# Performance work log

Measured on AMD Instinct MI355X. Metric: run time of the kernel, lower is better.

## Reference

```python
import jax, jax.numpy as jnp
import numpy as np

H = 32       # num query heads
KVH = 8      # num kv heads
HD = 64      # head_dim
ROPE_BASE = 10000.0


def _rope_cos_sin(seq_len, dtype):
    # inv_freq over half the head dim, emb = cat(freqs, freqs)
    inv_freq = 1.0 / (ROPE_BASE ** (jnp.arange(0, HD, 2, dtype=jnp.float32) / HD))
    t = jnp.arange(seq_len, dtype=jnp.float32)
    freqs = t[:, None] * inv_freq[None, :]          # (S, HD/2)
    emb = jnp.concatenate([freqs, freqs], axis=-1)  # (S, HD)
    return jnp.cos(emb).astype(dtype), jnp.sin(emb).astype(dtype)


def _rotate(x):
    x1, x2 = x[..., : HD // 2], x[..., HD // 2 :]
    return jnp.concatenate([-x2, x1], axis=-1)


def setup_inputs() -> dict:
    key = jax.random.key(0)
    ks = jax.random.split(key, 9)
    B, T, D = 2, 2048, 2048
    kv_dim = KVH * HD
    s = 0.02
    return {
        "x": jax.random.normal(ks[0], (B, T, D), jnp.float32),
        "Wq": jax.random.normal(ks[1], (D, D), jnp.float32) * s,
        "bq": jax.random.normal(ks[2], (D,), jnp.float32) * s,
        "Wk": jax.random.normal(ks[3], (kv_dim, D), jnp.float32) * s,
        "bk": jax.random.normal(ks[4], (kv_dim,), jnp.float32) * s,
        "Wv": jax.random.normal(ks[5], (kv_dim, D), jnp.float32) * s,
        "bv": jax.random.normal(ks[6], (kv_dim,), jnp.float32) * s,
        "Wo": jax.random.normal(ks[7], (D, D), jnp.float32) * s,
        "bo": jax.random.normal(ks[8], (D,), jnp.float32) * s,
    }


def reference(x, Wq, bq, Wk, bk, Wv, bv, Wo, bo):
    B, T, D = x.shape
    S = T  # self-attention, no KV cache (offset = 0)

    # QKV projections
    q = (x @ Wq.T + bq).reshape(B, T, H, HD)
    k = (x @ Wk.T + bk).reshape(B, S, KVH, HD)
    v = (x @ Wv.T + bv).reshape(B, S, KVH, HD)

    # RoPE (rotary dim == head_dim, offset 0)
    cos, sin = _rope_cos_sin(S, q.dtype)
    cos = cos[None, :, None, :]  # (1, S, 1, HD)
    sin = sin[None, :, None, :]
    q = q * cos + _rotate(q) * sin
    k = k * cos + _rotate(k) * sin

    # GQA: repeat kv heads (repeat_interleave along head dim)
    r = H // KVH
    k = jnp.repeat(k, r, axis=2)  # (B, S, H, HD)
    v = jnp.repeat(v, r, axis=2)

    # causal scaled dot-product attention
    scale = 1.0 / np.sqrt(HD)
    scores = jnp.einsum("bthd,bshd->bhts", q, k) * scale  # (B, H, T, S)
    causal = jnp.tril(jnp.ones((T, S), dtype=bool))
    scores = jnp.where(causal[None, None], scores, jnp.finfo(scores.dtype).min)
    probs = jax.nn.softmax(scores.astype(jnp.float32), axis=-1).astype(q.dtype)
    attn = jnp.einsum("bhts,bshd->bthd", probs, v)  # (B, T, H, HD)

    out = attn.reshape(B, T, H * HD) @ Wo.T + bo
    return out
```

## Files before the change

### kernel.cpp

```cpp
#include <hip/hip_runtime.h>
#include <hip/hip_bf16.h>
#include <cstdint>

#define B_ 2
#define T_ 2048
#define D_ 2048
#define H_ 32
#define KVH_ 8
#define HD_ 64
#define NQKV_ 3072
#define M_ 4096

typedef __attribute__((ext_vector_type(8))) __bf16 bf16x8;
typedef __attribute__((ext_vector_type(4))) float f32x4;
typedef __attribute__((ext_vector_type(4))) uint32_t u32x4;

__device__ __forceinline__ uint16_t f2bf(float f) {
  uint32_t u = __builtin_bit_cast(uint32_t, f);
  return (uint16_t)((u + 0x7FFFu + ((u >> 16) & 1u)) >> 16);
}

__device__ __forceinline__ uint32_t cvt_pk(float lo, float hi) {
  uint32_t r;
  asm("v_cvt_pk_bf16_f32 %0, %1, %2" : "=v"(r) : "v"(lo), "v"(hi));
  return r;
}

__device__ __forceinline__ void gload_lds16(const void* g, void* l) {
  __builtin_amdgcn_global_load_lds(
      (const __attribute__((address_space(1))) void*)(uintptr_t)g,
      (__attribute__((address_space(3))) void*)(uintptr_t)l, 16, 0, 0);
}

__global__ void cvt_bf16_k(const float* __restrict__ in, uint16_t* __restrict__ out, int n) {
  int i = (blockIdx.x * 256 + threadIdx.x) * 8;
  if (i >= n) return;
  float4 a = *reinterpret_cast<const float4*>(in + i);
  float4 b = *reinterpret_cast<const float4*>(in + i + 4);
  uint4 v;
  v.x = (uint32_t)f2bf(a.x) | ((uint32_t)f2bf(a.y) << 16);
  v.y = (uint32_t)f2bf(a.z) | ((uint32_t)f2bf(a.w) << 16);
  v.z = (uint32_t)f2bf(b.x) | ((uint32_t)f2bf(b.y) << 16);
  v.w = (uint32_t)f2bf(b.z) | ((uint32_t)f2bf(b.w) << 16);
  *reinterpret_cast<uint4*>(out + i) = v;
}

__global__ void concat_bias_k(const float* __restrict__ bq, const float* __restrict__ bk,
                              const float* __restrict__ bv, float* __restrict__ out) {
  int i = blockIdx.x * 256 + threadIdx.x;
  if (i >= NQKV_) return;
  out[i] = (i < D_) ? bq[i] : (i < D_ + 512) ? bk[i - D_] : bv[i - D_ - 512];
}

__global__ void rope_tab_k(float* __restrict__ cosT, float* __restrict__ sinT) {
  int i = blockIdx.x * 256 + threadIdx.x;
  int d = i & 31;
  int t = i >> 5;
  float inv = expf(-(float)d * (1.0f / 32.0f) * logf(10000.0f));
  float f = (float)t * inv;
  cosT[i] = cosf(f);
  sinT[i] = sinf(f);
}

#define BM 128
#define BN 128
#define BK 64
__global__ __launch_bounds__(256, 3)
void gemm_bf16(const uint16_t* __restrict__ A, const uint16_t* __restrict__ Bw,
               const float* __restrict__ bias, float* __restrict__ C,
               int M, int N, int K) {
  __shared__ __align__(16) uint16_t As[BM * BK];
  __shared__ __align__(16) uint16_t Bs[BN * BK];
  const int tid = threadIdx.x;
  const int lane = tid & 63;
  const int w = tid >> 6;
  const int wm = w >> 1, wn = w & 1;
  const int l16 = lane & 15, lq = lane >> 4;

  int lin = blockIdx.y * gridDim.x + blockIdx.x;
  int qn = (gridDim.x * gridDim.y) >> 3;
  int swz = (lin & 7) * qn + (lin >> 3);
  const int m0 = (swz / gridDim.x) * BM, n0 = (swz % gridDim.x) * BN;

  f32x4 acc[4][4] = {};

  for (int k0 = 0; k0 < K; k0 += BK) {
#pragma unroll
    for (int r = 0; r < 4; ++r) {
      int idx = r * 256 + tid;
      int row = idx >> 3;
      int c8 = (idx & 7) ^ (row & 7);
      gload_lds16(A + (size_t)(m0 + row) * K + k0 + c8 * 8, &As[idx * 8]);
    }
#pragma unroll
    for (int r = 0; r < 4; ++r) {
      int idx = r * 256 + tid;
      int row = idx >> 3;
      int c8 = (idx & 7) ^ (row & 7);
      gload_lds16(Bw + (size_t)(n0 + row) * K + k0 + c8 * 8, &Bs[idx * 8]);
    }
    __syncthreads();
#pragma unroll
    for (int ks = 0; ks < 2; ++ks) {
      bf16x8 av[4], bv[4];
      int k8 = ks * 4 + lq;
#pragma unroll
      for (int mi = 0; mi < 4; ++mi) {
        int row = wm * 64 + mi * 16 + l16;
        av[mi] = *reinterpret_cast<const bf16x8*>(&As[row * BK + ((k8 ^ (row & 7)) * 8)]);
      }
#pragma unroll
      for (int ni = 0; ni < 4; ++ni) {
        int row = wn * 64 + ni * 16 + l16;
        bv[ni] = *reinterpret_cast<const bf16x8*>(&Bs[row * BK + ((k8 ^ (row & 7)) * 8)]);
      }
#pragma unroll
      for (int mi = 0; mi < 4; ++mi)
#pragma unroll
        for (int ni = 0; ni < 4; ++ni)
          acc[mi][ni] = __builtin_amdgcn_mfma_f32_16x16x32_bf16(av[mi], bv[ni], acc[mi][ni], 0, 0, 0);
    }
    __syncthreads();
  }

#pragma unroll
  for (int mi = 0; mi < 4; ++mi) {
    int r0 = m0 + wm * 64 + mi * 16 + lq * 4;
#pragma unroll
    for (int ni = 0; ni < 4; ++ni) {
      int c = n0 + wn * 64 + ni * 16 + l16;
      float bb = bias[c];
#pragma unroll
      for (int rr = 0; rr < 4; ++rr)
        C[(size_t)(r0 + rr) * N + c] = acc[mi][ni][rr] + bb;
    }
  }
}

__global__ void rope_qk_k(const float* __restrict__ QKV, const float* __restrict__ cosT,
                          const float* __restrict__ sinT, uint16_t* __restrict__ qb,
                          uint16_t* __restrict__ kb) {
  int tid = blockIdx.x * 256 + threadIdx.x;
  int d = tid & 31;
  int t = (tid >> 5) & (T_ - 1);
  int rest = tid >> 16;
  int hh = rest % 40;
  int b = rest / 40;
  const float PREQ = 0.125f * 1.44269504f;
  float c = cosT[t * 32 + d];
  float s = sinT[t * 32 + d];
  size_t rowoff = (size_t)(b * T_ + t) * NQKV_;
  const int lq = d >> 3, e = d & 7;
  const int l16 = t & 15;
  const int lofs = (lq * 16 + l16) * 8 + e;
  if (hh < H_) {
    const float* q = QKV + rowoff + hh * 64;
    float x1 = q[d], x2 = q[d + 32];
    int tile = t >> 5, mf = (t >> 4) & 1;
    size_t base = ((size_t)(b * H_ + hh) * 64 + tile) * 2048;
    qb[base + (0 * 2 + mf) * 512 + lofs] = f2bf((x1 * c - x2 * s) * PREQ);
    qb[base + (1 * 2 + mf) * 512 + lofs] = f2bf((x2 * c + x1 * s) * PREQ);
  } else {
    int kh = hh - H_;
    const float* kp = QKV + rowoff + D_ + kh * 64;
    float x1 = kp[d], x2 = kp[d + 32];
    int it = t >> 6, nf = (t >> 4) & 3;
    size_t base = (size_t)(b * KVH_ + kh) * (T_ * HD_) + (size_t)it * 4096;
    kb[base + (0 * 8 + nf) * 512 + lofs] = f2bf(x1 * c - x2 * s);
    kb[base + (4 + nf) * 512 + lofs] = f2bf(x2 * c + x1 * s);
  }
}

__global__ void cvt_v_k(const float* __restrict__ QKV, uint16_t* __restrict__ vt) {
  int tid = blockIdx.x * 256 + threadIdx.x;
  int t8 = tid & 255;
  int rest = tid >> 8;
  int b = rest >> 9;
  int col = 2560 + (rest & 511);
  int d = rest & 63;
  int kvh = (rest >> 6) & 7;
  uint16_t tmp[8];
#pragma unroll
  for (int i = 0; i < 8; ++i)
    tmp[i] = f2bf(QKV[(size_t)(b * T_ + t8 * 8 + i) * NQKV_ + col]);
  uint4 v;
  v.x = (uint32_t)tmp[0] | ((uint32_t)tmp[1] << 16);
  v.y = (uint32_t)tmp[2] | ((uint32_t)tmp[3] << 16);
  v.z = (uint32_t)tmp[4] | ((uint32_t)tmp[5] << 16);
  v.w = (uint32_t)tmp[6] | ((uint32_t)tmp[7] << 16);
  int it = t8 >> 3, k2 = (t8 >> 2) & 1, lq = t8 & 3;
  int dn = d >> 4, l16 = d & 15;
  size_t base = (size_t)(b * KVH_ + kvh) * (T_ * HD_);
  *reinterpret_cast<uint4*>(vt + base + ((size_t)(it * 2 + k2) * 4 + dn) * 512 +
                            (lq * 16 + l16) * 8) = v;
}

__global__ __launch_bounds__(256, 2)
void flash_attn_k(const uint16_t* __restrict__ qb, const uint16_t* __restrict__ kb,
                  const uint16_t* __restrict__ vt, uint16_t* __restrict__ ob) {
  __shared__ __align__(16) uint16_t P_lds[4][32 * 72];
  const int lane = threadIdx.x & 63;
  const int w = threadIdx.x >> 6;
  const int l16 = lane & 15, lq = lane >> 4;
  const int bh = (blockIdx.x & 15) * 4 + w;
  const int rank = blockIdx.x >> 4;
  const int pair = rank & 31;
  const int tile = (rank & 32) ? (63 - pair) : pair;
  const int b = bh >> 5, h = bh & 31;
  const int kvh = h >> 2;
  uint16_t* P = P_lds[w];

  const uint16_t* Qp = qb + ((size_t)(b * H_ + h) * 64 + tile) * 2048;
  const uint16_t* Kp = kb + (size_t)(b * KVH_ + kvh) * (T_ * HD_);
  const uint16_t* Vp = vt + (size_t)(b * KVH_ + kvh) * (T_ * HD_);
  const int lofs = lane * 8;

  const int q0 = tile * 32;
  u32x4 ones_u = {0x3F803F80u, 0x3F803F80u, 0x3F803F80u, 0x3F803F80u};
  bf16x8 ones = __builtin_bit_cast(bf16x8, ones_u);

  bf16x8 aq[2][2];
#pragma unroll
  for (int mf = 0; mf < 2; ++mf)
#pragma unroll
    for (int ks = 0; ks < 2; ++ks)
      aq[mf][ks] = *reinterpret_cast<const bf16x8*>(Qp + (ks * 2 + mf) * 512 + lofs);

  f32x4 acc[2][4] = {};
  f32x4 acc_l[2] = {};

  const int nt = (tile >> 1) + 1;

  bf16x8 kA[2][4], kB[2][4];
#pragma unroll
  for (int ks = 0; ks < 2; ++ks)
#pragma unroll
    for (int nf = 0; nf < 4; ++nf)
      kA[ks][nf] = *reinterpret_cast<const bf16x8*>(Kp + (ks * 4 + nf) * 512 + lofs);

#define FLASH_STEP(KCUR, KNXT, IT)                                                     \
  do {                                                                                 \
    const int kv0 = (IT) * 64;                                                         \
    f32x4 sacc[4][2] = {};                                                             \
    _Pragma("unroll")                                                                  \
    for (int ks = 0; ks < 2; ++ks)                                                     \
      _Pragma("unroll")                                                                \
      for (int nf = 0; nf < 4; ++nf)                                                   \
        _Pragma("unroll")                                                              \
        for (int mf = 0; mf < 2; ++mf)                                                 \
          sacc[nf][mf] = __builtin_amdgcn_mfma_f32_16x16x32_bf16(                      \
              KCUR[ks][nf], aq[mf][ks], sacc[nf][mf], 0, 0, 0);                        \
    const int itn = ((IT) + 1 < nt) ? (IT) + 1 : (IT);                                 \
    _Pragma("unroll")                                                                  \
    for (int ks = 0; ks < 2; ++ks)                                                     \
      _Pragma("unroll")                                                                \
      for (int nf = 0; nf < 4; ++nf)                                                   \
        KNXT[ks][nf] = *reinterpret_cast<const bf16x8*>(                               \
            Kp + ((size_t)(itn * 2 + ks) * 4 + nf) * 512 + lofs);                      \
    bf16x8 vv[2][4];                                                                   \
    _Pragma("unroll")                                                                  \
    for (int k2 = 0; k2 < 2; ++k2)                                                     \
      _Pragma("unroll")                                                                \
      for (int dn = 0; dn < 4; ++dn)                                                   \
        vv[k2][dn] = *reinterpret_cast<const bf16x8*>(                                 \
            Vp + ((size_t)((IT) * 2 + k2) * 4 + dn) * 512 + lofs);                     \
    if ((IT) == nt - 1) {                                                              \
      _Pragma("unroll")                                                                \
      for (int mf = 0; mf < 2; ++mf) {                                                 \
        int qg = q0 + mf * 16 + l16;                                                   \
        _Pragma("unroll")                                                              \
        for (int nf = 0; nf < 4; ++nf)                                                 \
          _Pragma("unroll")                                                            \
          for (int r = 0; r < 4; ++r)                                                  \
            if (kv0 + nf * 16 + lq * 4 + r > qg) sacc[nf][mf][r] = -1e30f;             \
      }                                                                                \
    }                                                                                  \
    _Pragma("unroll")                                                                  \
    for (int mf = 0; mf < 2; ++mf) {                                                   \
      uint16_t* rowp = P + (mf * 16 + l16) * 72;                                       \
      _Pragma("unroll")                                                                \
      for (int nf = 0; nf < 4; ++nf) {                                                 \
        float p0 = __builtin_amdgcn_exp2f(sacc[nf][mf][0]);                            \
        float p1 = __builtin_amdgcn_exp2f(sacc[nf][mf][1]);                            \
        float p2 = __builtin_amdgcn_exp2f(sacc[nf][mf][2]);                            \
        float p3 = __builtin_amdgcn_exp2f(sacc[nf][mf][3]);                            \
        uint2 pk;                                                                      \
        pk.x = cvt_pk(p0, p1);                                                         \
        pk.y = cvt_pk(p2, p3);                                                         \
        *reinterpret_cast<uint2*>(rowp + nf * 16 + lq * 4) = pk;                       \
      }                                                                                \
    }                                                                                  \
    bf16x8 pa[2][2];                                                                   \
    _Pragma("unroll")                                                                  \
    for (int mf = 0; mf < 2; ++mf)                                                     \
      _Pragma("unroll")                                                                \
      for (int k2 = 0; k2 < 2; ++k2)                                                   \
        pa[mf][k2] = *reinterpret_cast<const bf16x8*>(                                 \
            P + (mf * 16 + l16) * 72 + k2 * 32 + lq * 8);                              \
    _Pragma("unroll")                                                                  \
    for (int k2 = 0; k2 < 2; ++k2)                                                     \
      _Pragma("unroll")                                                                \
      for (int mf = 0; mf < 2; ++mf) {                                                 \
        acc_l[mf] = __builtin_amdgcn_mfma_f32_16x16x32_bf16(ones, pa[mf][k2],          \
                                                            acc_l[mf], 0, 0, 0);      \
        _Pragma("unroll")                                                              \
        for (int dn = 0; dn < 4; ++dn)                                                 \
          acc[mf][dn] = __builtin_amdgcn_mfma_f32_16x16x32_bf16(                       \
              vv[k2][dn], pa[mf][k2], acc[mf][dn], 0, 0, 0);                           \
      }                                                                                \
  } while (0)

  {
    int it = 0;
    for (;;) {
      FLASH_STEP(kA, kB, it);
      ++it;
      if (it == nt) break;
      FLASH_STEP(kB, kA, it);
      ++it;
      if (it == nt) break;
    }
  }
#undef FLASH_STEP

#pragma unroll
  for (int mf = 0; mf < 2; ++mf) {
    float inv = 1.0f / acc_l[mf][0];
    uint16_t* rowp = P + (mf * 16 + l16) * 72;
#pragma unroll
    for (int dn = 0; dn < 4; ++dn) {
      uint2 pk;
      pk.x = cvt_pk(acc[mf][dn][0] * inv, acc[mf][dn][1] * inv);
      pk.y = cvt_pk(acc[mf][dn][2] * inv, acc[mf][dn][3] * inv);
      *reinterpret_cast<uint2*>(rowp + dn * 16 + lq * 4) = pk;
    }
  }
  {
    int orow = lane >> 1, ohalf = (lane & 1) * 32;
    uint16_t* op = ob + (size_t)(b * T_ + q0 + orow) * D_ + h * HD_ + ohalf;
    const uint16_t* lp = P + orow * 72 + ohalf;
#pragma unroll
    for (int j = 0; j < 4; ++j)
      *reinterpret_cast<uint4*>(op + j * 8) = *reinterpret_cast<const uint4*>(lp + j * 8);
  }
}

extern "C" void kernel_launch(void* const* d_in, const int* in_sizes, int n_in,
                              void* d_out, int out_size, void* d_ws, size_t ws_size,
                              hipStream_t stream) {
  const float* x  = (const float*)d_in[0];
  const float* Wq = (const float*)d_in[1];
  const float* bq = (const float*)d_in[2];
  const float* Wk = (const float*)d_in[3];
  const float* bk = (const float*)d_in[4];
  const float* Wv = (const float*)d_in[5];
  const float* bv = (const float*)d_in[6];
  const float* Wo = (const float*)d_in[7];
  const float* bo = (const float*)d_in[8];
  float* out = (float*)d_out;

  char* ws = (char*)d_ws;
  size_t off = 0;
  auto alloc = [&](size_t bytes) {
    void* p = ws + off;
    off += (bytes + 255) & ~(size_t)255;
    return p;
  };
  uint16_t* xb    = (uint16_t*)alloc((size_t)M_ * D_ * 2);
  uint16_t* wqkv  = (uint16_t*)alloc((size_t)NQKV_ * D_ * 2);
  uint16_t* wo_b  = (uint16_t*)alloc((size_t)D_ * D_ * 2);
  float*    bqkv  = (float*)alloc(NQKV_ * 4);
  float*    cosT  = (float*)alloc(T_ * 32 * 4);
  float*    sinT  = (float*)alloc(T_ * 32 * 4);
  uint16_t* q_bf  = (uint16_t*)alloc((size_t)B_ * H_ * T_ * HD_ * 2);
  uint16_t* k_bf  = (uint16_t*)alloc((size_t)B_ * KVH_ * T_ * HD_ * 2);
  uint16_t* vt_bf = (uint16_t*)alloc((size_t)B_ * KVH_ * T_ * HD_ * 2);
  float*    qkvf  = (float*)alloc((size_t)M_ * NQKV_ * 4);
  uint16_t* attn_bf = (uint16_t*)qkvf;

  cvt_bf16_k<<<4096, 256, 0, stream>>>(x, xb, M_ * D_);
  cvt_bf16_k<<<2048, 256, 0, stream>>>(Wq, wqkv, D_ * D_);
  cvt_bf16_k<<<512, 256, 0, stream>>>(Wk, wqkv + (size_t)D_ * D_, 512 * D_);
  cvt_bf16_k<<<512, 256, 0, stream>>>(Wv, wqkv + (size_t)2560 * D_, 512 * D_);
  cvt_bf16_k<<<2048, 256, 0, stream>>>(Wo, wo_b, D_ * D_);
  concat_bias_k<<<12, 256, 0, stream>>>(bq, bk, bv, bqkv);
  rope_tab_k<<<256, 256, 0, stream>>>(cosT, sinT);

  gemm_bf16<<<dim3(NQKV_ / BN, M_ / BM), 256, 0, stream>>>(xb, wqkv, bqkv, qkvf, M_, NQKV_, D_);

  rope_qk_k<<<(B_ * 40 * T_ * 32) / 256, 256, 0, stream>>>(qkvf, cosT, sinT, q_bf, k_bf);
  cvt_v_k<<<(B_ * KVH_ * HD_ * (T_ / 8)) / 256, 256, 0, stream>>>(qkvf, vt_bf);

  flash_attn_k<<<1024, 256, 0, stream>>>(q_bf, k_bf, vt_bf, attn_bf);

  gemm_bf16<<<dim3(D_ / BN, M_ / BM), 256, 0, stream>>>(attn_bf, wo_b, bo, out, M_, D_, D_);
}
```

Before: 206.0 us.

## Store QKV projection in bf16 and transpose V through shared memory

The QKV GEMM now writes its biased output as bf16 instead of fp32, which halves the intermediate buffer's write and read traffic. The RoPE and V-layout kernels read bf16 directly. The V transpose kernel is rewritten to load coalesced 64x64 tiles into LDS and emit packed vectors from there, replacing strided scalar global reads. Rounding Q/K to bf16 before RoPE adds a small extra rounding step compared with the fp32 path.

Result: faster. 189.0 us (-8.3%).

```diff
diff --git a/kernel.cpp b/kernel.cpp
--- a/kernel.cpp
+++ b/kernel.cpp
@@ -18,6 +18,10 @@
 __device__ __forceinline__ uint16_t f2bf(float f) {
   uint32_t u = __builtin_bit_cast(uint32_t, f);
   return (uint16_t)((u + 0x7FFFu + ((u >> 16) & 1u)) >> 16);
+}
+
+__device__ __forceinline__ float bf2f(uint16_t u) {
+  return __builtin_bit_cast(float, (uint32_t)u << 16);
 }
 
 __device__ __forceinline__ uint32_t cvt_pk(float lo, float hi) {
@@ -65,9 +69,10 @@
 #define BM 128
 #define BN 128
 #define BK 64
+template <bool OUTBF16>
 __global__ __launch_bounds__(256, 3)
 void gemm_bf16(const uint16_t* __restrict__ A, const uint16_t* __restrict__ Bw,
-               const float* __restrict__ bias, float* __restrict__ C,
+               const float* __restrict__ bias, void* __restrict__ Cv,
                int M, int N, int K) {
   __shared__ __align__(16) uint16_t As[BM * BK];
   __shared__ __align__(16) uint16_t Bs[BN * BK];
@@ -131,13 +136,18 @@
       int c = n0 + wn * 64 + ni * 16 + l16;
       float bb = bias[c];
 #pragma unroll
-      for (int rr = 0; rr < 4; ++rr)
-        C[(size_t)(r0 + rr) * N + c] = acc[mi][ni][rr] + bb;
-    }
-  }
-}
-
-__global__ void rope_qk_k(const float* __restrict__ QKV, const float* __restrict__ cosT,
+      for (int rr = 0; rr < 4; ++rr) {
+        float v = acc[mi][ni][rr] + bb;
+        if constexpr (OUTBF16)
+          ((uint16_t*)Cv)[(size_t)(r0 + rr) * N + c] = f2bf(v);
+        else
+          ((float*)Cv)[(size_t)(r0 + rr) * N + c] = v;
+      }
+    }
+  }
+}
+
+__global__ void rope_qk_k(const uint16_t* __restrict__ QKV, const float* __restrict__ cosT,
                           const float* __restrict__ sinT, uint16_t* __restrict__ qb,
                           uint16_t* __restrict__ kb) {
   int tid = blockIdx.x * 256 + threadIdx.x;
@@ -154,16 +164,16 @@
   const int l16 = t & 15;
   const int lofs = (lq * 16 + l16) * 8 + e;
   if (hh < H_) {
-    const float* q = QKV + rowoff + hh * 64;
-    float x1 = q[d], x2 = q[d + 32];
+    const uint16_t* q = QKV + rowoff + hh * 64;
+    float x1 = bf2f(q[d]), x2 = bf2f(q[d + 32]);
     int tile = t >> 5, mf = (t >> 4) & 1;
     size_t base = ((size_t)(b * H_ + hh) * 64 + tile) * 2048;
     qb[base + (0 * 2 + mf) * 512 + lofs] = f2bf((x1 * c - x2 * s) * PREQ);
     qb[base + (1 * 2 + mf) * 512 + lofs] = f2bf((x2 * c + x1 * s) * PREQ);
   } else {
     int kh = hh - H_;
-    const float* kp = QKV + rowoff + D_ + kh * 64;
-    float x1 = kp[d], x2 = kp[d + 32];
+    const uint16_t* kp = QKV + rowoff + D_ + kh * 64;
+    float x1 = bf2f(kp[d]), x2 = bf2f(kp[d + 32]);
     int it = t >> 6, nf = (t >> 4) & 3;
     size_t base = (size_t)(b * KVH_ + kh) * (T_ * HD_) + (size_t)it * 4096;
     kb[base + (0 * 8 + nf) * 512 + lofs] = f2bf(x1 * c - x2 * s);
@@ -171,28 +181,45 @@
   }
 }
 
-__global__ void cvt_v_k(const float* __restrict__ QKV, uint16_t* __restrict__ vt) {
-  int tid = blockIdx.x * 256 + threadIdx.x;
-  int t8 = tid & 255;
-  int rest = tid >> 8;
-  int b = rest >> 9;
-  int col = 2560 + (rest & 511);
-  int d = rest & 63;
-  int kvh = (rest >> 6) & 7;
-  uint16_t tmp[8];
-#pragma unroll
-  for (int i = 0; i < 8; ++i)
-    tmp[i] = f2bf(QKV[(size_t)(b * T_ + t8 * 8 + i) * NQKV_ + col]);
-  uint4 v;
-  v.x = (uint32_t)tmp[0] | ((uint32_t)tmp[1] << 16);
-  v.y = (uint32_t)tmp[2] | ((uint32_t)tmp[3] << 16);
-  v.z = (uint32_t)tmp[4] | ((uint32_t)tmp[5] << 16);
-  v.w = (uint32_t)tmp[6] | ((uint32_t)tmp[7] << 16);
-  int it = t8 >> 3, k2 = (t8 >> 2) & 1, lq = t8 & 3;
+__global__ void cvt_v_k(const uint16_t* __restrict__ QKV, uint16_t* __restrict__ vt) {
+  __shared__ uint16_t tile[64][72];
+  int blk = blockIdx.x;
+  int it = blk & 31;
+  int kvh = (blk >> 5) & 7;
+  int b = blk >> 8;
+  int tid = threadIdx.x;
+  int t0 = it * 64;
+
+  {
+    int r = tid >> 2;
+    int cg = (tid & 3) * 16;
+    const uint16_t* src = QKV + (size_t)(b * T_ + t0 + r) * NQKV_ + 2560 + kvh * 64 + cg;
+    uint4 v0 = *reinterpret_cast<const uint4*>(src);
+    uint4 v1 = *reinterpret_cast<const uint4*>(src + 8);
+    *reinterpret_cast<uint4*>(&tile[r][cg]) = v0;
+    *reinterpret_cast<uint4*>(&tile[r][cg + 8]) = v1;
+  }
+  __syncthreads();
+
+  int d = tid & 63;
+  int wv = tid >> 6;
   int dn = d >> 4, l16 = d & 15;
   size_t base = (size_t)(b * KVH_ + kvh) * (T_ * HD_);
-  *reinterpret_cast<uint4*>(vt + base + ((size_t)(it * 2 + k2) * 4 + dn) * 512 +
-                            (lq * 16 + l16) * 8) = v;
+#pragma unroll
+  for (int j = 0; j < 2; ++j) {
+    int oct = wv * 2 + j;
+    int k2 = oct >> 2, lq = oct & 3;
+    uint16_t tmp[8];
+#pragma unroll
+    for (int e = 0; e < 8; ++e) tmp[e] = tile[oct * 8 + e][d];
+    uint4 v;
+    v.x = (uint32_t)tmp[0] | ((uint32_t)tmp[1] << 16);
+    v.y = (uint32_t)tmp[2] | ((uint32_t)tmp[3] << 16);
+    v.z = (uint32_t)tmp[4] | ((uint32_t)tmp[5] << 16);
+    v.w = (uint32_t)tmp[6] | ((uint32_t)tmp[7] << 16);
+    *reinterpret_cast<uint4*>(vt + base + ((size_t)(it * 2 + k2) * 4 + dn) * 512 +
+                              (lq * 16 + l16) * 8) = v;
+  }
 }
 
 __global__ __launch_bounds__(256, 2)
@@ -375,8 +402,8 @@
   uint16_t* q_bf  = (uint16_t*)alloc((size_t)B_ * H_ * T_ * HD_ * 2);
   uint16_t* k_bf  = (uint16_t*)alloc((size_t)B_ * KVH_ * T_ * HD_ * 2);
   uint16_t* vt_bf = (uint16_t*)alloc((size_t)B_ * KVH_ * T_ * HD_ * 2);
-  float*    qkvf  = (float*)alloc((size_t)M_ * NQKV_ * 4);
-  uint16_t* attn_bf = (uint16_t*)qkvf;
+  uint16_t* qkv_bf = (uint16_t*)alloc((size_t)M_ * NQKV_ * 2);
+  uint16_t* attn_bf = qkv_bf;
 
   cvt_bf16_k<<<4096, 256, 0, stream>>>(x, xb, M_ * D_);
   cvt_bf16_k<<<2048, 256, 0, stream>>>(Wq, wqkv, D_ * D_);
@@ -386,12 +413,14 @@
   concat_bias_k<<<12, 256, 0, stream>>>(bq, bk, bv, bqkv);
   rope_tab_k<<<256, 256, 0, stream>>>(cosT, sinT);
 
-  gemm_bf16<<<dim3(NQKV_ / BN, M_ / BM), 256, 0, stream>>>(xb, wqkv, bqkv, qkvf, M_, NQKV_, D_);
-
-  rope_qk_k<<<(B_ * 40 * T_ * 32) / 256, 256, 0, stream>>>(qkvf, cosT, sinT, q_bf, k_bf);
-  cvt_v_k<<<(B_ * KVH_ * HD_ * (T_ / 8)) / 256, 256, 0, stream>>>(qkvf, vt_bf);
+  gemm_bf16<true><<<dim3(NQKV_ / BN, M_ / BM), 256, 0, stream>>>(
+      xb, wqkv, bqkv, qkv_bf, M_, NQKV_, D_);
+
+  rope_qk_k<<<(B_ * 40 * T_ * 32) / 256, 256, 0, stream>>>(qkv_bf, cosT, sinT, q_bf, k_bf);
+  cvt_v_k<<<B_ * KVH_ * (T_ / 64), 256, 0, stream>>>(qkv_bf, vt_bf);
 
   flash_attn_k<<<1024, 256, 0, stream>>>(q_bf, k_bf, vt_bf, attn_bf);
 
-  gemm_bf16<<<dim3(D_ / BN, M_ / BM), 256, 0, stream>>>(attn_bf, wo_b, bo, out, M_, D_, D_);
-}
+  gemm_bf16<false><<<dim3(D_ / BN, M_ / BM), 256, 0, stream>>>(
+      attn_bf, wo_b, bo, out, M_, D_, D_);
+}
```
